# Performance work log

Measured on AMD Instinct MI355X. Metric: run time of the kernel, lower is better.

Reference implementation:

```python
import jax, jax.numpy as jnp
import numpy as np

HIDDEN = 512
HEADS = 8
DHEAD = HIDDEN // HEADS  # 64


def setup_inputs() -> dict:
    key = jax.random.key(0)
    ks = jax.random.split(key, 12)
    B, S = 2, 2048
    inp = {
        "q": jax.random.normal(ks[0], (B, S, HIDDEN), dtype=jnp.float32),
        "k": jax.random.normal(ks[1], (B, S, HIDDEN), dtype=jnp.float32),
        "v": jax.random.normal(ks[2], (B, S, HIDDEN), dtype=jnp.float32),
        "mask": jnp.zeros((B, 1, 1, S), dtype=bool),
    }
    scale = 1.0 / np.sqrt(HIDDEN)
    for i, name in enumerate(["Wq", "Wk", "Wv", "Wm"]):
        inp[name] = jax.random.normal(ks[3 + i], (HIDDEN, HIDDEN), dtype=jnp.float32) * scale
    for i, name in enumerate(["bq", "bk", "bv", "bm"]):
        inp[name] = jax.random.normal(ks[7 + i], (HIDDEN,), dtype=jnp.float32) * 0.01
    return inp


def reference(q, k, v, mask, Wq, Wk, Wv, Wm, bq, bk, bv, bm):
    B = q.shape[0]
    # Linear projections (torch Linear: x @ W.T + b)
    qh = (jnp.einsum("bsd,ed->bse", q, Wq) + bq).reshape(B, HEADS, -1, DHEAD)
    kh = (jnp.einsum("bsd,ed->bse", k, Wk) + bk).reshape(B, HEADS, -1, DHEAD)
    vh = (jnp.einsum("bsd,ed->bse", v, Wv) + bv).reshape(B, HEADS, -1, DHEAD)
    # NOTE: the original module reshapes [B,S,512] -> [B,8,S',64] directly
    # (splitting the sequence dim into heads, not the hidden dim); replicated here.
    s = jnp.einsum("bhqd,bhkd->bhqk", qh, kh) / jnp.sqrt(jnp.float32(DHEAD))
    s = jnp.where(mask, jnp.float32(-1e9), s)
    s = jax.nn.softmax(s, axis=-1)
    # dropout is identity in eval mode
    attn = jnp.einsum("bhqk,bhkd->bhqd", s, vh)  # [B,H,S',64]
    attn = attn.transpose(0, 2, 1, 3).reshape(B, -1, HIDDEN)
    return jnp.einsum("bsd,ed->bse", attn, Wm) + bm
```

## Files before the change

### kernel.cpp

```cpp
#include <hip/hip_runtime.h>
#include <hip/hip_bf16.h>
#include <math.h>

typedef float  f32x4 __attribute__((ext_vector_type(4)));
typedef short  s16x8 __attribute__((ext_vector_type(8)));
typedef short  s16x4 __attribute__((ext_vector_type(4)));
typedef unsigned short u16x4 __attribute__((ext_vector_type(4)));

__device__ inline unsigned short bfc(float f){
  __hip_bfloat16 h = __float2bfloat16(f);
  unsigned short u; __builtin_memcpy(&u, &h, 2); return u;
}

__device__ inline f32x4 mfma16(s16x4 a, s16x4 b, f32x4 c){
#if __has_builtin(__builtin_amdgcn_mfma_f32_16x16x16_bf16)
  return __builtin_amdgcn_mfma_f32_16x16x16_bf16(a, b, c, 0, 0, 0);
#elif __has_builtin(__builtin_amdgcn_mfma_f32_16x16x16bf16_1k)
  return __builtin_amdgcn_mfma_f32_16x16x16bf16_1k(a, b, c, 0, 0, 0);
#else
  asm("v_mfma_f32_16x16x16_bf16 %0, %1, %2, %0" : "+v"(c) : "v"(a), "v"(b));
  return c;
#endif
}

__device__ inline void gl_lds16(const unsigned short* g, unsigned short* l){
  __builtin_amdgcn_global_load_lds(
      (const __attribute__((address_space(1))) unsigned int*)g,
      (__attribute__((address_space(3))) unsigned int*)l, 16, 0, 0);
}

__global__ __launch_bounds__(256) void prep(const float* __restrict__ q, const float* __restrict__ k,
                                            const float* __restrict__ v,
                                            const float* __restrict__ w0, const float* __restrict__ w1,
                                            const float* __restrict__ w2, const float* __restrict__ w3,
                                            const unsigned char* __restrict__ mask,
                                            unsigned short* __restrict__ AP, unsigned short* __restrict__ WP,
                                            float* __restrict__ mf){
  int y = blockIdx.y;
  int t = blockIdx.x * 256 + threadIdx.x;
  if (y < 3){
    const float* src = y==0 ? q : (y==1 ? k : v);
    unsigned short* d = AP + (size_t)y * 2097152;
    int r = t >> 6, g = t & 63;
    const float* sp = src + (size_t)r * 512 + g * 8;
    f32x4 a0 = *(const f32x4*)sp;
    f32x4 a1 = *(const f32x4*)(sp + 4);
    s16x8 o = { (short)bfc(a0.x),(short)bfc(a0.y),(short)bfc(a0.z),(short)bfc(a0.w),
                (short)bfc(a1.x),(short)bfc(a1.y),(short)bfc(a1.z),(short)bfc(a1.w) };
    size_t off = ((size_t)(((r>>4)*16 + (g>>2))*64 + (g&3)*16 + (r&15))) * 8;
    *(s16x8*)(d + off) = o;
  } else if (y < 7){
    if (blockIdx.x < 128){
      int yy = y - 3;
      const float* src = yy==0 ? w0 : yy==1 ? w1 : yy==2 ? w2 : w3;
      int c = t >> 6, g = t & 63;
      const float* sp = src + (size_t)c * 512 + g * 8;
      f32x4 a0 = *(const f32x4*)sp;
      f32x4 a1 = *(const f32x4*)(sp + 4);
      s16x8 o = { (short)bfc(a0.x),(short)bfc(a0.y),(short)bfc(a0.z),(short)bfc(a0.w),
                  (short)bfc(a1.x),(short)bfc(a1.y),(short)bfc(a1.z),(short)bfc(a1.w) };
      size_t off = ((size_t)(((c>>4)*16 + (g>>2))*64 + (g&3)*16 + (c&15))) * 8;
      *(s16x8*)(WP + yy*262144 + off) = o;
    }
  } else if (t < 4096){
    mf[t] = mask[t] ? -1.442695e9f : 0.0f;
  }
}

__global__ __launch_bounds__(256) void proj_gemm(const unsigned short* __restrict__ Ap,
    const unsigned short* __restrict__ Wp,
    const float* __restrict__ bq, const float* __restrict__ bk, const float* __restrict__ bv,
    unsigned short* __restrict__ pout){
  int z = blockIdx.z;
  const unsigned short* A = Ap + (size_t)z * 2097152;
  const unsigned short* W = Wp + (size_t)z * 262144;
  const float* bias = z==0 ? bq : (z==1 ? bk : bv);
  unsigned short* out = pout + (size_t)z * 2097152;

  int w = threadIdx.x >> 6, lane = threadIdx.x & 63;
  int lr = lane & 15, lg = lane >> 4;
  int rt = blockIdx.x * 4 + w;
  int bn = blockIdx.y;

  f32x4 acc[4] = {};
  const unsigned short* Abase = A + ((size_t)rt*8192 + lane*8);
  const unsigned short* Wbase = W + ((size_t)bn*32768 + lane*8);
#pragma unroll 4
  for (int kc = 0; kc < 16; ++kc){
    s16x8 af = *(const s16x8*)(Abase + kc*512);
#pragma unroll
    for (int n = 0; n < 4; ++n){
      s16x8 bf = *(const s16x8*)(Wbase + ((size_t)n*16 + kc)*512);
      acc[n] = __builtin_amdgcn_mfma_f32_16x16x32_bf16(af, bf, acc[n], 0, 0, 0);
    }
  }
  int orow = rt*16 + lg*4;
#pragma unroll
  for (int n = 0; n < 4; ++n){
    int col = bn*64 + n*16 + lr;
    float bv_ = bias[col];
#pragma unroll
    for (int r = 0; r < 4; ++r)
      out[(size_t)(orow + r)*512 + col] = bfc(acc[n][r] + bv_);
  }
}

__global__ __launch_bounds__(256) void vtrans(const unsigned short* __restrict__ Pv,
                                              unsigned short* __restrict__ Vt){
  int kt = blockIdx.x, bh = blockIdx.y;
  int b = bh >> 3, h = bh & 7;
  __shared__ unsigned short t[64][65];
  const unsigned short* src = Pv + (size_t)(b*2048 + h*256)*512 + kt*4096;
  for (int i = threadIdx.x; i < 4096; i += 256){ int r = i >> 6, c = i & 63; t[r][c] = src[i]; }
  __syncthreads();
  unsigned short* dst = Vt + (size_t)bh*131072 + kt*64;
  for (int i = threadIdx.x; i < 4096; i += 256){ int d = i >> 6, kk = i & 63; dst[(size_t)d*2048 + kk] = t[kk][d]; }
}

__global__ __launch_bounds__(512, 4) void flash(const unsigned short* __restrict__ Pq,
                                             const unsigned short* __restrict__ Pk,
                                             const unsigned short* __restrict__ Vt,
                                             const float* __restrict__ mf,
                                             unsigned short* __restrict__ aout){
  int qt = blockIdx.x;
  int bh = blockIdx.y;
  int b = bh >> 3, h = bh & 7;
  int w = threadIdx.x >> 6;
  int wq = w & 1, wk = w >> 1;
  int lane = threadIdx.x & 63;
  int lr = lane & 15, lg = lane >> 4;

  const unsigned short* Qh  = Pq + (size_t)(b*2048 + h*256)*512;
  const unsigned short* Kh  = Pk + (size_t)(b*2048 + h*256)*512 + (size_t)wk*32768;
  const unsigned short* Vth = Vt + (size_t)bh*131072 + wk*512;
  const float* mp = mf + b*2048 + wk*512 + lg*4;

  __shared__ char smem[65536];
  unsigned short* ktile = (unsigned short*)smem;
  unsigned short* vtile = (unsigned short*)(smem + 32768);
  float* obuf = (float*)smem;
  float* lbuf = (float*)(smem + 49152);

  int krow_l = lane >> 3;
  int cxor  = (lane & 7) ^ krow_l;
  int kcol_l = cxor * 8;

  int vhalf32 = (cxor >> 2) * 32;
  int vkc = (cxor & 3) * 8;
  const unsigned short* kg0 = Kh + (size_t)(8*(wq*2+0) + krow_l)*64 + kcol_l;
  const unsigned short* kg1 = Kh + (size_t)(8*(wq*2+1) + krow_l)*64 + kcol_l;
  const unsigned short* vg0 = Vth + (size_t)(wq*16 + 0 + krow_l + vhalf32)*2048 + vkc;
  const unsigned short* vg1 = Vth + (size_t)(wq*16 + 8 + krow_l + vhalf32)*2048 + vkc;

  s16x8 qf[2][2];
#pragma unroll
  for (int qq = 0; qq < 2; ++qq){
    int qrow = qt*64 + wq*32 + qq*16 + lr;
    qf[qq][0] = *(const s16x8*)(Qh + (size_t)qrow*64 + lg*8);
    qf[qq][1] = *(const s16x8*)(Qh + (size_t)qrow*64 + 32 + lg*8);
  }

  float l[2] = {0.f, 0.f};
  f32x4 accT[2][4] = {};
  int kswz = (lr & 7) * 16;

#define STAGE(dbuf) { \
    unsigned short* kd = ktile + ((dbuf)*4 + wk)*2048; \
    unsigned short* vd = vtile + ((dbuf)*4 + wk)*2048; \
    gl_lds16(kg0, kd + (wq*2+0)*512); \
    gl_lds16(kg1, kd + (wq*2+1)*512); \
    gl_lds16(vg0, vd + (wq*2+0)*512); \
    gl_lds16(vg1, vd + (wq*2+1)*512); \
    kg0 += 2048; kg1 += 2048; vg0 += 32; vg1 += 32; }

  STAGE(0)
  __syncthreads();
  int cur = 0;

  for (int t = 0; t < 16; ++t){
    if (t < 15) STAGE(cur ^ 1)

    const char* kb = (const char*)(ktile + (cur*4 + wk)*2048);
    const char* vb = (const char*)(vtile + (cur*4 + wk)*2048);

    float s2[2][2][4];
    __builtin_amdgcn_s_setprio(1);
#pragma unroll
    for (int n = 0; n < 2; ++n){
      int krow = n*16 + lr;
      s16x8 kf0 = *(const s16x8*)(kb + krow*128 + ((lg*16) ^ kswz));
      s16x8 kf1 = *(const s16x8*)(kb + krow*128 + ((64 + lg*16) ^ kswz));
      f32x4 mv = *(const f32x4*)(mp + n*16);
#pragma unroll
      for (int qq = 0; qq < 2; ++qq){
        f32x4 a = {};
        a = __builtin_amdgcn_mfma_f32_16x16x32_bf16(kf0, qf[qq][0], a, 0, 0, 0);
        a = __builtin_amdgcn_mfma_f32_16x16x32_bf16(kf1, qf[qq][1], a, 0, 0, 0);
#pragma unroll
        for (int r = 0; r < 4; ++r)
          s2[qq][n][r] = __builtin_fmaf(a[r], 0.18033688f, mv[r]);
      }
    }
    __builtin_amdgcn_s_setprio(0);

    s16x4 pf[2][2];
#pragma unroll
    for (int qq = 0; qq < 2; ++qq){
#pragma unroll
      for (int n = 0; n < 2; ++n){
        float p0 = __builtin_amdgcn_exp2f(s2[qq][n][0]);
        float p1 = __builtin_amdgcn_exp2f(s2[qq][n][1]);
        float p2 = __builtin_amdgcn_exp2f(s2[qq][n][2]);
        float p3 = __builtin_amdgcn_exp2f(s2[qq][n][3]);
        l[qq] += (p0 + p1) + (p2 + p3);
        pf[qq][n] = (s16x4){ (short)bfc(p0), (short)bfc(p1), (short)bfc(p2), (short)bfc(p3) };
      }
    }

    __builtin_amdgcn_s_setprio(1);
#pragma unroll
    for (int n = 0; n < 2; ++n){
#pragma unroll
      for (int nd = 0; nd < 4; ++nd){
        int vrow = (nd & 1)*16 + lr;
        int vchunk = ((nd >> 1)*4 + n*2 + (lg >> 1)) ^ (vrow & 7);
        s16x4 vf = *(const s16x4*)(vb + vrow*128 + vchunk*16 + (lg & 1)*8);
        accT[0][nd] = mfma16(vf, pf[0][n], accT[0][nd]);
        accT[1][nd] = mfma16(vf, pf[1][n], accT[1][nd]);
      }
    }
    __builtin_amdgcn_s_setprio(0);

    mp += 32;
    __syncthreads();
    cur ^= 1;
  }
#undef STAGE

  float lt[2];
#pragma unroll
  for (int qq = 0; qq < 2; ++qq){
    float x = l[qq] + __shfl_xor(l[qq], 16);
    lt[qq] = x + __shfl_xor(x, 32);
  }

  if (wk != 0){
    int j = wk - 1;
#pragma unroll
    for (int qq = 0; qq < 2; ++qq){
      int reg = j*4 + wq*2 + qq;
      if (lg == 0) lbuf[reg*16 + lr] = lt[qq];
#pragma unroll
      for (int nd = 0; nd < 4; ++nd)
        *(f32x4*)&obuf[((size_t)reg*64 + lane)*16 + nd*4] = accT[qq][nd];
    }
  }
  __syncthreads();
  if (wk == 0){
#pragma unroll
    for (int qq = 0; qq < 2; ++qq){
      float ltot = lt[qq];
#pragma unroll
      for (int j = 0; j < 3; ++j)
        ltot += lbuf[(j*4 + wq*2 + qq)*16 + lr];
      float inv = (ltot > 0.f) ? 1.f / ltot : 0.f;
      int q = qt*64 + wq*32 + qq*16 + lr;
      int rt = (b*2048 + q) >> 4;
#pragma unroll
      for (int nd = 0; nd < 4; ++nd){
        f32x4 o = accT[qq][nd];
#pragma unroll
        for (int j = 0; j < 3; ++j){
          int reg = j*4 + wq*2 + qq;
          f32x4 oj = *(const f32x4*)&obuf[((size_t)reg*64 + lane)*16 + nd*4];
          o += oj;
        }
        int g = h*8 + nd*2 + (lg >> 1);
        u16x4 ov = { bfc(o[0]*inv), bfc(o[1]*inv), bfc(o[2]*inv), bfc(o[3]*inv) };
        unsigned short* dp = aout + ((size_t)((rt*16 + (g>>2))*64 + (g&3)*16 + lr))*8 + (lg&1)*4;
        *(u16x4*)dp = ov;
      }
    }
  }
}

__global__ __launch_bounds__(256) void gemm_out(const unsigned short* __restrict__ Ap,
                                                const unsigned short* __restrict__ Wp,
                                                const float* __restrict__ bias,
                                                float* __restrict__ out){
  int w = threadIdx.x >> 6, lane = threadIdx.x & 63;
  int lr = lane & 15, lg = lane >> 4;
  int rt = blockIdx.x * 4 + w;
  int bn = blockIdx.y;
  f32x4 acc[4] = {};
  const unsigned short* Abase = Ap + ((size_t)rt*8192 + lane*8);
  const unsigned short* Wbase = Wp + ((size_t)bn*32768 + lane*8);
#pragma unroll 4
  for (int kc = 0; kc < 16; ++kc){
    s16x8 af = *(const s16x8*)(Abase + kc*512);
#pragma unroll
    for (int n = 0; n < 4; ++n){
      s16x8 bf = *(const s16x8*)(Wbase + ((size_t)n*16 + kc)*512);
      acc[n] = __builtin_amdgcn_mfma_f32_16x16x32_bf16(af, bf, acc[n], 0, 0, 0);
    }
  }
  int orow = rt*16 + lg*4;
#pragma unroll
  for (int n = 0; n < 4; ++n){
    int col = bn*64 + n*16 + lr;
    float bv_ = bias[col];
#pragma unroll
    for (int r = 0; r < 4; ++r)
      out[(size_t)(orow + r)*512 + col] = acc[n][r] + bv_;
  }
}

extern "C" void kernel_launch(void* const* d_in, const int* in_sizes, int n_in,
                              void* d_out, int out_size, void* d_ws, size_t ws_size,
                              hipStream_t stream) {
  const float* q  = (const float*)d_in[0];
  const float* k  = (const float*)d_in[1];
  const float* v  = (const float*)d_in[2];
  const unsigned char* mask = (const unsigned char*)d_in[3];
  const float* Wq = (const float*)d_in[4];
  const float* Wk = (const float*)d_in[5];
  const float* Wv = (const float*)d_in[6];
  const float* Wm = (const float*)d_in[7];
  const float* bq = (const float*)d_in[8];
  const float* bk = (const float*)d_in[9];
  const float* bv = (const float*)d_in[10];
  const float* bm = (const float*)d_in[11];

  unsigned short* ws = (unsigned short*)d_ws;
  unsigned short* WP   = ws;
  float*          MF   = (float*)(ws + 1048576);
  unsigned short* AP   = ws + 1056768;
  unsigned short* PQ   = ws + 7348224;
  unsigned short* VT   = ws + 13639680;
  unsigned short* AO   = ws + 15736832;

  prep<<<dim3(1024, 8), 256, 0, stream>>>(q, k, v, Wq, Wk, Wv, Wm, mask, AP, WP, MF);
  proj_gemm<<<dim3(64, 8, 3), 256, 0, stream>>>(AP, WP, bq, bk, bv, PQ);
  vtrans<<<dim3(32, 16), 256, 0, stream>>>(PQ + 2*2097152, VT);
  flash<<<dim3(32, 16), 512, 0, stream>>>(PQ, PQ + 2097152, VT, MF, AO);
  gemm_out<<<dim3(64, 8), 256, 0, stream>>>(AO, WP + 3*262144, bm, (float*)d_out);
}
```

Baseline: 77.68 us.

## Fuse V transpose into projection GEMM epilogue and prefetch mask values

The V projection epilogue now writes its output directly in transposed per-head layout, so the separate vtrans kernel launch and its read/write round trip through global memory go away. The flash kernel also loads the mask values for the next key tile one iteration ahead, taking that global load latency off the critical path. The transposed stores are strided (stride 8 elements along keys, 2048 across rows), which may coalesce poorly compared with the original row-major stores.

```diff
diff --git a/kernel.cpp b/kernel.cpp
--- a/kernel.cpp
+++ b/kernel.cpp
@@ -70,7 +70,7 @@
 __global__ __launch_bounds__(256) void proj_gemm(const unsigned short* __restrict__ Ap,
     const unsigned short* __restrict__ Wp,
     const float* __restrict__ bq, const float* __restrict__ bk, const float* __restrict__ bv,
-    unsigned short* __restrict__ pout){
+    unsigned short* __restrict__ pout, unsigned short* __restrict__ Vt){
   int z = blockIdx.z;
   const unsigned short* A = Ap + (size_t)z * 2097152;
   const unsigned short* W = Wp + (size_t)z * 262144;
@@ -94,27 +94,30 @@
       acc[n] = __builtin_amdgcn_mfma_f32_16x16x32_bf16(af, bf, acc[n], 0, 0, 0);
     }
   }
-  int orow = rt*16 + lg*4;
-#pragma unroll
-  for (int n = 0; n < 4; ++n){
-    int col = bn*64 + n*16 + lr;
-    float bv_ = bias[col];
-#pragma unroll
-    for (int r = 0; r < 4; ++r)
-      out[(size_t)(orow + r)*512 + col] = bfc(acc[n][r] + bv_);
-  }
-}
-
-__global__ __launch_bounds__(256) void vtrans(const unsigned short* __restrict__ Pv,
-                                              unsigned short* __restrict__ Vt){
-  int kt = blockIdx.x, bh = blockIdx.y;
-  int b = bh >> 3, h = bh & 7;
-  __shared__ unsigned short t[64][65];
-  const unsigned short* src = Pv + (size_t)(b*2048 + h*256)*512 + kt*4096;
-  for (int i = threadIdx.x; i < 4096; i += 256){ int r = i >> 6, c = i & 63; t[r][c] = src[i]; }
-  __syncthreads();
-  unsigned short* dst = Vt + (size_t)bh*131072 + kt*64;
-  for (int i = threadIdx.x; i < 4096; i += 256){ int d = i >> 6, kk = i & 63; dst[(size_t)d*2048 + kk] = t[kk][d]; }
+  if (z < 2){
+    int orow = rt*16 + lg*4;
+#pragma unroll
+    for (int n = 0; n < 4; ++n){
+      int col = bn*64 + n*16 + lr;
+      float bv_ = bias[col];
+#pragma unroll
+      for (int r = 0; r < 4; ++r)
+        out[(size_t)(orow + r)*512 + col] = bfc(acc[n][r] + bv_);
+    }
+  } else {
+    int bh = (rt >> 7) * 8 + ((rt >> 4) & 7);
+    int keyb = ((rt & 15)*16 + lg*4) * 8 + bn;
+    unsigned short* vt = Vt + (size_t)bh * 131072;
+#pragma unroll
+    for (int n = 0; n < 4; ++n){
+      int col = bn*64 + n*16 + lr;
+      float bv_ = bias[col];
+      unsigned short* vp = vt + (size_t)(n*16 + lr) * 2048 + keyb;
+#pragma unroll
+      for (int r = 0; r < 4; ++r)
+        vp[r*8] = bfc(acc[n][r] + bv_);
+    }
+  }
 }
 
 __global__ __launch_bounds__(512, 4) void flash(const unsigned short* __restrict__ Pq,
@@ -174,11 +177,20 @@
     kg0 += 2048; kg1 += 2048; vg0 += 32; vg1 += 32; }
 
   STAGE(0)
+  f32x4 cmv0 = *(const f32x4*)(mp);
+  f32x4 cmv1 = *(const f32x4*)(mp + 16);
+  mp += 32;
   __syncthreads();
   int cur = 0;
 
   for (int t = 0; t < 16; ++t){
     if (t < 15) STAGE(cur ^ 1)
+    f32x4 nmv0, nmv1;
+    if (t < 15){
+      nmv0 = *(const f32x4*)(mp);
+      nmv1 = *(const f32x4*)(mp + 16);
+      mp += 32;
+    }
 
     const char* kb = (const char*)(ktile + (cur*4 + wk)*2048);
     const char* vb = (const char*)(vtile + (cur*4 + wk)*2048);
@@ -190,7 +202,7 @@
       int krow = n*16 + lr;
       s16x8 kf0 = *(const s16x8*)(kb + krow*128 + ((lg*16) ^ kswz));
       s16x8 kf1 = *(const s16x8*)(kb + krow*128 + ((64 + lg*16) ^ kswz));
-      f32x4 mv = *(const f32x4*)(mp + n*16);
+      f32x4 mv = n ? cmv1 : cmv0;
 #pragma unroll
       for (int qq = 0; qq < 2; ++qq){
         f32x4 a = {};
@@ -231,7 +243,7 @@
     }
     __builtin_amdgcn_s_setprio(0);
 
-    mp += 32;
+    cmv0 = nmv0; cmv1 = nmv1;
     __syncthreads();
     cur ^= 1;
   }
@@ -340,8 +352,7 @@
   unsigned short* AO   = ws + 15736832;
 
   prep<<<dim3(1024, 8), 256, 0, stream>>>(q, k, v, Wq, Wk, Wv, Wm, mask, AP, WP, MF);
-  proj_gemm<<<dim3(64, 8, 3), 256, 0, stream>>>(AP, WP, bq, bk, bv, PQ);
-  vtrans<<<dim3(32, 16), 256, 0, stream>>>(PQ + 2*2097152, VT);
+  proj_gemm<<<dim3(64, 8, 3), 256, 0, stream>>>(AP, WP, bq, bk, bv, PQ, VT);
   flash<<<dim3(32, 16), 512, 0, stream>>>(PQ, PQ + 2097152, VT, MF, AO);
   gemm_out<<<dim3(64, 8), 256, 0, stream>>>(AO, WP + 3*262144, bm, (float*)d_out);
 }
```

Measured after the change: 86.13 us. 10.9% more time.
